# Kernel optimization log

Measured on AMD Instinct MI355X. Metric: run time of the kernel, lower is better.

Reference implementation:

```python
import jax, jax.numpy as jnp
import numpy as np

N, E, F, K = 20000, 320000, 256, 3


def setup_inputs() -> dict:
    key = jax.random.key(0)
    ks = jax.random.split(key, 10)
    x = jax.random.normal(ks[0], (N, F), jnp.float32)
    edge_index = jax.random.randint(ks[1], (2, E), 0, N)
    edge_weight = jax.random.uniform(ks[2], (E,), jnp.float32)
    h = jax.random.normal(ks[3], (N, F), jnp.float32)
    c = jax.random.normal(ks[4], (N, F), jnp.float32)
    s = 1.0 / np.sqrt(F)
    W = jax.random.normal(ks[5], (4, F, F), jnp.float32) * s        # x->gate (i,f,c,o)
    theta = jax.random.normal(ks[6], (4, K, F, F), jnp.float32) * s  # Cheb weights per gate
    b_conv = jnp.zeros((4, F), jnp.float32)                          # ChebConv biases
    b = jnp.zeros((4, F), jnp.float32)                               # gate biases
    w_c = jax.random.normal(ks[7], (3, F), jnp.float32) * s          # peephole (i,f,o)
    W_cls = jax.random.normal(ks[8], (F, 1), jnp.float32) * s
    b_cls = jnp.zeros((1,), jnp.float32)
    return dict(x=x, edge_index=edge_index, edge_weight=edge_weight, h=h, c=c,
                W=W, theta=theta, b_conv=b_conv, b=b, w_c=w_c, W_cls=W_cls, b_cls=b_cls)


def _cheb(h, src, dst, wnorm, theta_g, b_g):
    # ChebConv with sym normalization, lambda_max=2: L_hat = -D^{-1/2} A D^{-1/2}
    n = h.shape[0]

    def prop(v):  # (L_hat v)[dst] = sum_e wnorm[e] * v[src[e]]
        return jax.ops.segment_sum(wnorm[:, None] * v[src], dst, num_segments=n)

    Tx0 = h
    out = Tx0 @ theta_g[0]
    Tx1 = prop(h)
    out = out + Tx1 @ theta_g[1]
    for k in range(2, theta_g.shape[0]):
        Tx2 = 2.0 * prop(Tx1) - Tx0
        out = out + Tx2 @ theta_g[k]
        Tx0, Tx1 = Tx1, Tx2
    return out + b_g


def _gclstm(x, src, dst, wnorm, h, c, W, theta, b_conv, b, w_c):
    conv = lambda g: _cheb(h, src, dst, wnorm, theta[g], b_conv[g])
    i = jax.nn.sigmoid(x @ W[0] + conv(0) + w_c[0] * c + b[0])
    f = jax.nn.sigmoid(x @ W[1] + conv(1) + w_c[1] * c + b[1])
    t = jnp.tanh(x @ W[2] + conv(2) + b[2])
    c_new = f * c + i * t
    o = jax.nn.sigmoid(x @ W[3] + conv(3) + w_c[2] * c_new + b[3])
    h_new = o * jnp.tanh(c_new)
    return h_new, c_new


def reference(x, edge_index, edge_weight, h, c, W, theta, b_conv, b, w_c, W_cls, b_cls):
    src, dst = edge_index[0], edge_index[1]
    deg = jax.ops.segment_sum(edge_weight, src, num_segments=x.shape[0])
    dis = jnp.where(deg > 0, jax.lax.rsqrt(jnp.maximum(deg, 1e-12)), 0.0)
    wnorm = -dis[src] * edge_weight * dis[dst]
    h0, c0 = _gclstm(x, src, dst, wnorm, h, c, W, theta, b_conv, b, w_c)
    out = jax.nn.relu(h0) @ W_cls + b_cls  # [N, 1]
    return out, h0, c0
```

## Files before the change

### kernel.cpp

```cpp
#include <hip/hip_runtime.h>
#include <stdint.h>

#define FDIM 256
#define KDIM 1024

typedef __attribute__((ext_vector_type(8))) short short8;
typedef __attribute__((ext_vector_type(4))) float floatx4;

#define GLOBAL_AS __attribute__((address_space(1)))
#define LDS_AS    __attribute__((address_space(3)))

static __device__ __forceinline__ unsigned short f2bf(float f) {
    unsigned int u = __float_as_uint(f);
    unsigned int r = (u + 0x7FFFu + ((u >> 16) & 1u)) >> 16;
    return (unsigned short)r;
}
static __device__ __forceinline__ float bf2f(unsigned short s) {
    return __uint_as_float(((unsigned int)s) << 16);
}
static __device__ __forceinline__ float sig(float x) {
    return 1.f / (1.f + __expf(-x));
}


__global__ void k_degcnt(const int* __restrict__ src, const int* __restrict__ dst,
                         const float* __restrict__ ew, float* deg, int* cnt, int e) {
    int i = blockIdx.x * blockDim.x + threadIdx.x;
    if (i < e) {
        atomicAdd(&deg[src[i]], ew[i]);
        atomicAdd(&cnt[dst[i]], 1);
    }
}

__global__ void k_dis(const float* __restrict__ deg, float* __restrict__ dis, int n) {
    int i = blockIdx.x * blockDim.x + threadIdx.x;
    if (i < n) {
        float d = deg[i];
        dis[i] = d > 0.f ? rsqrtf(fmaxf(d, 1e-12f)) : 0.f;
    }
}

__launch_bounds__(1024)
__global__ void k_scan1(const int* __restrict__ cnt, int* __restrict__ offs,
                        int* __restrict__ part, int n) {
    __shared__ int wsum[16];
    int b = blockIdx.x;
    int i = b * 1024 + (int)threadIdx.x;
    int lane = threadIdx.x & 63;
    int wid = threadIdx.x >> 6;
    int x = (i < n) ? cnt[i] : 0;
#pragma unroll
    for (int s = 1; s < 64; s <<= 1) {
        int t = __shfl_up(x, s);
        if (lane >= s) x += t;
    }
    if (lane == 63) wsum[wid] = x;
    __syncthreads();
    if (wid == 0) {
        int y = (lane < 16) ? wsum[lane] : 0;
#pragma unroll
        for (int s = 1; s < 16; s <<= 1) {
            int t = __shfl_up(y, s);
            if (lane >= s) y += t;
        }
        if (lane < 16) wsum[lane] = y;
    }
    __syncthreads();
    int wbase = (wid > 0) ? wsum[wid - 1] : 0;
    if (i < n) offs[i + 1] = wbase + x;
    if (threadIdx.x == 1023) part[b] = wsum[15];
}

__launch_bounds__(1024)
__global__ void k_scan2(int* __restrict__ offs, const int* __restrict__ part, int n) {
    __shared__ int sprefix;
    int b = blockIdx.x;
    if (threadIdx.x < 64) {
        int p = ((int)threadIdx.x < b) ? part[threadIdx.x] : 0;
#pragma unroll
        for (int s = 32; s; s >>= 1) p += __shfl_down(p, s);
        if (threadIdx.x == 0) sprefix = p;
    }
    __syncthreads();
    int i = b * 1024 + (int)threadIdx.x;
    if (i < n) offs[i + 1] += sprefix;
    if (b == 0 && threadIdx.x == 0) offs[0] = 0;
}

__global__ void k_scatter(const int* __restrict__ src, const int* __restrict__ dst,
                          const float* __restrict__ ew, const float* __restrict__ dis,
                          const int* __restrict__ offs, int* cur,
                          int* __restrict__ csr_src, float* __restrict__ csr_w, int e) {
    int i = blockIdx.x * blockDim.x + threadIdx.x;
    if (i < e) {
        int s = src[i], d = dst[i];
        float wn = -dis[s] * ew[i] * dis[d];
        int pos = offs[d] + atomicAdd(&cur[d], 1);
        csr_src[pos] = s;
        csr_w[pos] = wn;
    }
}


__global__ void k_packA(const float* __restrict__ x, const float* __restrict__ h,
                        unsigned short* __restrict__ A, int n) {
    int t = blockIdx.x * blockDim.x + threadIdx.x;
    int node = t >> 6, q = t & 63;
    if (node >= n) return;
    floatx4 xv = *(const floatx4*)(x + (size_t)node * FDIM + q * 4);
    floatx4 hv = *(const floatx4*)(h + (size_t)node * FDIM + q * 4);
    ushort4 ox, oh;
    ox.x = f2bf(xv[0]); ox.y = f2bf(xv[1]); ox.z = f2bf(xv[2]); ox.w = f2bf(xv[3]);
    oh.x = f2bf(hv[0]); oh.y = f2bf(hv[1]); oh.z = f2bf(hv[2]); oh.w = f2bf(hv[3]);
    *(ushort4*)(A + (size_t)node * KDIM + q * 4) = ox;
    *(ushort4*)(A + (size_t)node * KDIM + FDIM + q * 4) = oh;
}

__global__ void k_packBt(const float* __restrict__ W, const float* __restrict__ theta,
                         unsigned short* __restrict__ Bt) {
    int t = blockIdx.x * blockDim.x + threadIdx.x;
    int p = t >> 10, r = t & 1023;
    int group = p >> 6, gate = (p >> 4) & 3;
    int feat = (group << 4) | (p & 15);
    int kb = r >> 8, rr = r & 255;
    float v;
    if (kb == 0) v = W[((size_t)(gate * FDIM + rr)) * FDIM + feat];
    else         v = theta[((size_t)((gate * 3 + (kb - 1)) * FDIM + rr)) * FDIM + feat];
    Bt[t] = f2bf(v);
}


__launch_bounds__(256)
__global__ void k_prop1(unsigned short* __restrict__ A, const int* __restrict__ offs,
                        const int* __restrict__ csr_src, const float* __restrict__ csr_w, int n) {
    int wid = (blockIdx.x * blockDim.x + threadIdx.x) >> 6;
    int lane = threadIdx.x & 63;
    if (wid >= n) return;
    int half = lane >> 5, l = lane & 31;
    int beg = offs[wid], end = offs[wid + 1];
    float a[8] = {0.f, 0.f, 0.f, 0.f, 0.f, 0.f, 0.f, 0.f};
    int j = beg + half;
    for (; j + 2 < end; j += 4) {
        int s0 = csr_src[j], s1 = csr_src[j + 2];
        float w0 = csr_w[j], w1 = csr_w[j + 2];
        short8 v0 = *(const short8*)(A + (size_t)s0 * KDIM + FDIM + l * 8);
        short8 v1 = *(const short8*)(A + (size_t)s1 * KDIM + FDIM + l * 8);
#pragma unroll
        for (int k = 0; k < 8; ++k)
            a[k] += w0 * bf2f((unsigned short)v0[k]) + w1 * bf2f((unsigned short)v1[k]);
    }
    if (j < end) {
        int s0 = csr_src[j];
        float w0 = csr_w[j];
        short8 v0 = *(const short8*)(A + (size_t)s0 * KDIM + FDIM + l * 8);
#pragma unroll
        for (int k = 0; k < 8; ++k) a[k] += w0 * bf2f((unsigned short)v0[k]);
    }
#pragma unroll
    for (int k = 0; k < 8; ++k) a[k] += __shfl_xor(a[k], 32);
    if (half == 0) {
        short8 o;
#pragma unroll
        for (int k = 0; k < 8; ++k) o[k] = (short)f2bf(a[k]);
        *(short8*)(A + (size_t)wid * KDIM + 2 * FDIM + l * 8) = o;
    }
}

__launch_bounds__(256)
__global__ void k_prop2(unsigned short* __restrict__ A, const float* __restrict__ h,
                        const int* __restrict__ offs,
                        const int* __restrict__ csr_src, const float* __restrict__ csr_w, int n) {
    int wid = (blockIdx.x * blockDim.x + threadIdx.x) >> 6;
    int lane = threadIdx.x & 63;
    if (wid >= n) return;
    int half = lane >> 5, l = lane & 31;
    int beg = offs[wid], end = offs[wid + 1];
    float a[8] = {0.f, 0.f, 0.f, 0.f, 0.f, 0.f, 0.f, 0.f};
    int j = beg + half;
    for (; j + 2 < end; j += 4) {
        int s0 = csr_src[j], s1 = csr_src[j + 2];
        float w0 = csr_w[j], w1 = csr_w[j + 2];
        short8 v0 = *(const short8*)(A + (size_t)s0 * KDIM + 2 * FDIM + l * 8);
        short8 v1 = *(const short8*)(A + (size_t)s1 * KDIM + 2 * FDIM + l * 8);
#pragma unroll
        for (int k = 0; k < 8; ++k)
            a[k] += w0 * bf2f((unsigned short)v0[k]) + w1 * bf2f((unsigned short)v1[k]);
    }
    if (j < end) {
        int s0 = csr_src[j];
        float w0 = csr_w[j];
        short8 v0 = *(const short8*)(A + (size_t)s0 * KDIM + 2 * FDIM + l * 8);
#pragma unroll
        for (int k = 0; k < 8; ++k) a[k] += w0 * bf2f((unsigned short)v0[k]);
    }
#pragma unroll
    for (int k = 0; k < 8; ++k) a[k] += __shfl_xor(a[k], 32);
    if (half == 0) {
        floatx4 hv0 = *(const floatx4*)(h + (size_t)wid * FDIM + l * 8);
        floatx4 hv1 = *(const floatx4*)(h + (size_t)wid * FDIM + l * 8 + 4);
        short8 o;
#pragma unroll
        for (int k = 0; k < 4; ++k) o[k] = (short)f2bf(2.f * a[k] - hv0[k]);
#pragma unroll
        for (int k = 0; k < 4; ++k) o[4 + k] = (short)f2bf(2.f * a[4 + k] - hv1[k]);
        *(short8*)(A + (size_t)wid * KDIM + 3 * FDIM + l * 8) = o;
    }
}


__launch_bounds__(256, 3)
__global__ void k_gemm(const unsigned short* __restrict__ A, const unsigned short* __restrict__ Bt,
                       const float* __restrict__ c, const float* __restrict__ b_conv,
                       const float* __restrict__ b, const float* __restrict__ w_c,
                       const float* __restrict__ Wcls,
                       float* __restrict__ out_h, float* __restrict__ out_c,
                       float* __restrict__ cls_part, int M, int mtiles) {
    __shared__ unsigned short sA[128 * 64];
    __shared__ unsigned short sB[128 * 64];
    int tid = threadIdx.x;
    int lane = tid & 63;
    int w = tid >> 6;
    int nb = mtiles * 8;
    int bid = blockIdx.x;
    int wg = (bid & 7) * (nb >> 3) + (bid >> 3);
    int mt = wg >> 3;
    int nt = wg & 7;
    int brow = mt * 128, bcol = nt * 128;
    int wr = (w >> 1) * 64, wc = (w & 1) * 64;
    int l15 = lane & 15, l4 = lane >> 4;

    floatx4 acc[4][4];
#pragma unroll
    for (int m = 0; m < 4; ++m)
#pragma unroll
        for (int g = 0; g < 4; ++g)
            acc[m][g] = (floatx4){0.f, 0.f, 0.f, 0.f};

    for (int kt = 0; kt < 16; ++kt) {
        int k0 = kt * 64;
#pragma unroll
        for (int p = 0; p < 4; ++p) {
            int cch = tid + p * 256;
            int row = cch >> 3, cslot = cch & 7;
            int csrc = cslot ^ (row & 7);
            int grow = brow + row; if (grow >= M) grow = M - 1;
            const unsigned short* g = A + (size_t)grow * KDIM + k0 + csrc * 8;
            __builtin_amdgcn_global_load_lds((const GLOBAL_AS void*)g,
                                             (LDS_AS void*)(sA + cch * 8), 16, 0, 0);
        }
#pragma unroll
        for (int p = 0; p < 4; ++p) {
            int cch = tid + p * 256;
            int row = cch >> 3, cslot = cch & 7;
            int csrc = cslot ^ (row & 7);
            const unsigned short* g = Bt + (size_t)(bcol + row) * KDIM + k0 + csrc * 8;
            __builtin_amdgcn_global_load_lds((const GLOBAL_AS void*)g,
                                             (LDS_AS void*)(sB + cch * 8), 16, 0, 0);
        }
        __syncthreads();

#pragma unroll
        for (int ks = 0; ks < 2; ++ks) {
            short8 af[4], bfr[4];
#pragma unroll
            for (int m = 0; m < 4; ++m) {
                int ra = wr + m * 16 + l15;
                af[m] = *(const short8*)(sA + ra * 64 + ((ks * 4 + l4) ^ (ra & 7)) * 8);
            }
#pragma unroll
            for (int g = 0; g < 4; ++g) {
                int rb = wc + g * 16 + l15;
                bfr[g] = *(const short8*)(sB + rb * 64 + ((ks * 4 + l4) ^ (rb & 7)) * 8);
            }
#pragma unroll
            for (int m = 0; m < 4; ++m)
#pragma unroll
                for (int g = 0; g < 4; ++g)
                    acc[m][g] = __builtin_amdgcn_mfma_f32_16x16x32_bf16(af[m], bfr[g], acc[m][g], 0, 0, 0);
        }
        __syncthreads();
    }

    int group = (bcol + wc) >> 6;
    int feat = (group << 4) | l15;
    float bc0 = b_conv[feat], bc1 = b_conv[FDIM + feat];
    float bc2 = b_conv[2 * FDIM + feat], bc3 = b_conv[3 * FDIM + feat];
    float bb0 = b[feat], bb1 = b[FDIM + feat];
    float bb2 = b[2 * FDIM + feat], bb3 = b[3 * FDIM + feat];
    float wci = w_c[feat], wcf = w_c[FDIM + feat], wco = w_c[2 * FDIM + feat];
    float wcl = Wcls[feat];

#pragma unroll
    for (int m = 0; m < 4; ++m) {
#pragma unroll
        for (int j = 0; j < 4; ++j) {
            int node = brow + wr + m * 16 + l4 * 4 + j;
            bool ok = node < M;
            int nidx = ok ? node : (M - 1);
            float cv = c[(size_t)nidx * FDIM + feat];
            float iv = sig(acc[m][0][j] + bc0 + wci * cv + bb0);
            float fv = sig(acc[m][1][j] + bc1 + wcf * cv + bb1);
            float tv = tanhf(acc[m][2][j] + bc2 + bb2);
            float cn = fv * cv + iv * tv;
            float ov = sig(acc[m][3][j] + bc3 + wco * cn + bb3);
            float hn = ov * tanhf(cn);
            if (ok) {
                out_h[(size_t)node * FDIM + feat] = hn;
                out_c[(size_t)node * FDIM + feat] = cn;
            }
            float pcls = fmaxf(hn, 0.f) * wcl;
#pragma unroll
            for (int s = 1; s < 16; s <<= 1) pcls += __shfl_xor(pcls, s);
            if (ok && l15 == 0) cls_part[(size_t)node * 16 + group] = pcls;
        }
    }
}

__global__ void k_cls(const float* __restrict__ cls_part, const float* __restrict__ bcls,
                      float* __restrict__ out_cls, int n) {
    int i = blockIdx.x * blockDim.x + threadIdx.x;
    if (i >= n) return;
    const floatx4* p = (const floatx4*)(cls_part + (size_t)i * 16);
    floatx4 v0 = p[0], v1 = p[1], v2 = p[2], v3 = p[3];
    float s = v0[0] + v0[1] + v0[2] + v0[3] + v1[0] + v1[1] + v1[2] + v1[3]
            + v2[0] + v2[1] + v2[2] + v2[3] + v3[0] + v3[1] + v3[2] + v3[3];
    out_cls[i] = s + bcls[0];
}


extern "C" void kernel_launch(void* const* d_in, const int* in_sizes, int n_in,
                              void* d_out, int out_size, void* d_ws, size_t ws_size,
                              hipStream_t stream) {
    const float* x      = (const float*)d_in[0];
    const int*   eidx   = (const int*)d_in[1];
    const float* ew     = (const float*)d_in[2];
    const float* h      = (const float*)d_in[3];
    const float* c      = (const float*)d_in[4];
    const float* W      = (const float*)d_in[5];
    const float* theta  = (const float*)d_in[6];
    const float* b_conv = (const float*)d_in[7];
    const float* b      = (const float*)d_in[8];
    const float* w_c    = (const float*)d_in[9];
    const float* Wcls   = (const float*)d_in[10];
    const float* bcls   = (const float*)d_in[11];

    const int N = in_sizes[0] / FDIM;
    const int E = in_sizes[2];
    const int* src = eidx;
    const int* dst = eidx + E;

    char* ws = (char*)d_ws;
    size_t off = 0;
    auto alloc = [&](size_t bytes) -> void* {
        void* p = ws + off;
        off += (bytes + 255) & ~(size_t)255;
        return p;
    };
    unsigned short* A   = (unsigned short*)alloc((size_t)N * KDIM * 2);
    unsigned short* Bt  = (unsigned short*)alloc((size_t)KDIM * KDIM * 2);
    float* cls_part     = (float*)alloc((size_t)N * 16 * 4);
    float* deg          = (float*)alloc((size_t)N * 4);
    int*   cnt          = (int*)alloc((size_t)N * 4);
    int*   cur          = (int*)alloc((size_t)N * 4);
    float* dis          = (float*)alloc((size_t)N * 4);
    int*   offs         = (int*)alloc((size_t)(N + 1) * 4);
    int*   part         = (int*)alloc(64 * 4);
    int*   csr_src      = (int*)alloc((size_t)E * 4);
    float* csr_w        = (float*)alloc((size_t)E * 4);
    (void)ws_size; (void)n_in; (void)out_size;

    float* out_cls = (float*)d_out;
    float* out_h   = out_cls + N;
    float* out_c   = out_h + (size_t)N * FDIM;

    size_t zbytes = (size_t)((char*)(cur + N) - (char*)deg);
    hipMemsetAsync(deg, 0, zbytes, stream);

    int nsb = (N + 1023) / 1024;
    k_degcnt<<<(E + 255) / 256, 256, 0, stream>>>(src, dst, ew, deg, cnt, E);
    k_dis<<<(N + 255) / 256, 256, 0, stream>>>(deg, dis, N);
    k_scan1<<<nsb, 1024, 0, stream>>>(cnt, offs, part, N);
    k_scan2<<<nsb, 1024, 0, stream>>>(offs, part, N);
    k_scatter<<<(E + 255) / 256, 256, 0, stream>>>(src, dst, ew, dis, offs, cur, csr_src, csr_w, E);
    k_packA<<<(N * 64 + 255) / 256, 256, 0, stream>>>(x, h, A, N);
    k_packBt<<<(KDIM * KDIM + 255) / 256, 256, 0, stream>>>(W, theta, Bt);
    k_prop1<<<(N * 64 + 255) / 256, 256, 0, stream>>>(A, offs, csr_src, csr_w, N);
    k_prop2<<<(N * 64 + 255) / 256, 256, 0, stream>>>(A, h, offs, csr_src, csr_w, N);
    int mtiles = (N + 127) / 128;
    k_gemm<<<mtiles * 8, 256, 0, stream>>>(A, Bt, c, b_conv, b, w_c, Wcls,
                                           out_h, out_c, cls_part, N, mtiles);
    k_cls<<<(N + 255) / 256, 256, 0, stream>>>(cls_part, bcls, out_cls, N);
}
```

Before: 200.6 us.

## Double-buffer GEMM LDS tiles, pack CSR as int2, unroll gathers, fold rsqrt into scatter

The GEMM kernel now stages the next K tile into a second LDS buffer while computing on the current one, using explicit vmcnt waits and raw barriers, and drops its occupancy hint from 3 to 2 blocks. Source index and weight are packed into one int2 CSR array so each edge is a single load. The prop kernels are unrolled to four gathers per half-wave. The separate dis kernel is removed and the rsqrt is computed inside the scatter. Together these aim to hide global-to-LDS latency and cut launch and memory traffic, at the cost of twice the LDS per block and lower occupancy in the GEMM.

```diff
diff --git a/kernel.cpp b/kernel.cpp
--- a/kernel.cpp
+++ b/kernel.cpp
@@ -29,14 +29,6 @@
     if (i < e) {
         atomicAdd(&deg[src[i]], ew[i]);
         atomicAdd(&cnt[dst[i]], 1);
-    }
-}
-
-__global__ void k_dis(const float* __restrict__ deg, float* __restrict__ dis, int n) {
-    int i = blockIdx.x * blockDim.x + threadIdx.x;
-    if (i < n) {
-        float d = deg[i];
-        dis[i] = d > 0.f ? rsqrtf(fmaxf(d, 1e-12f)) : 0.f;
     }
 }
 
@@ -88,16 +80,18 @@
 }
 
 __global__ void k_scatter(const int* __restrict__ src, const int* __restrict__ dst,
-                          const float* __restrict__ ew, const float* __restrict__ dis,
+                          const float* __restrict__ ew, const float* __restrict__ deg,
                           const int* __restrict__ offs, int* cur,
-                          int* __restrict__ csr_src, float* __restrict__ csr_w, int e) {
+                          int2* __restrict__ csr, int e) {
     int i = blockIdx.x * blockDim.x + threadIdx.x;
     if (i < e) {
         int s = src[i], d = dst[i];
-        float wn = -dis[s] * ew[i] * dis[d];
+        float ds_ = deg[s], dd = deg[d];
+        float rs = ds_ > 0.f ? rsqrtf(fmaxf(ds_, 1e-12f)) : 0.f;
+        float rd = dd > 0.f ? rsqrtf(fmaxf(dd, 1e-12f)) : 0.f;
+        float wn = -rs * ew[i] * rd;
         int pos = offs[d] + atomicAdd(&cur[d], 1);
-        csr_src[pos] = s;
-        csr_w[pos] = wn;
+        csr[pos] = make_int2(s, __float_as_int(wn));
     }
 }
 
@@ -132,7 +126,7 @@
 
 __launch_bounds__(256)
 __global__ void k_prop1(unsigned short* __restrict__ A, const int* __restrict__ offs,
-                        const int* __restrict__ csr_src, const float* __restrict__ csr_w, int n) {
+                        const int2* __restrict__ csr, int n) {
     int wid = (blockIdx.x * blockDim.x + threadIdx.x) >> 6;
     int lane = threadIdx.x & 63;
     if (wid >= n) return;
@@ -140,19 +134,23 @@
     int beg = offs[wid], end = offs[wid + 1];
     float a[8] = {0.f, 0.f, 0.f, 0.f, 0.f, 0.f, 0.f, 0.f};
     int j = beg + half;
-    for (; j + 2 < end; j += 4) {
-        int s0 = csr_src[j], s1 = csr_src[j + 2];
-        float w0 = csr_w[j], w1 = csr_w[j + 2];
-        short8 v0 = *(const short8*)(A + (size_t)s0 * KDIM + FDIM + l * 8);
-        short8 v1 = *(const short8*)(A + (size_t)s1 * KDIM + FDIM + l * 8);
+    for (; j + 6 < end; j += 8) {
+        int2 e0 = csr[j], e1 = csr[j + 2], e2 = csr[j + 4], e3 = csr[j + 6];
+        short8 v0 = *(const short8*)(A + (size_t)e0.x * KDIM + FDIM + l * 8);
+        short8 v1 = *(const short8*)(A + (size_t)e1.x * KDIM + FDIM + l * 8);
+        short8 v2 = *(const short8*)(A + (size_t)e2.x * KDIM + FDIM + l * 8);
+        short8 v3 = *(const short8*)(A + (size_t)e3.x * KDIM + FDIM + l * 8);
+        float w0 = __int_as_float(e0.y), w1 = __int_as_float(e1.y);
+        float w2 = __int_as_float(e2.y), w3 = __int_as_float(e3.y);
 #pragma unroll
         for (int k = 0; k < 8; ++k)
-            a[k] += w0 * bf2f((unsigned short)v0[k]) + w1 * bf2f((unsigned short)v1[k]);
-    }
-    if (j < end) {
-        int s0 = csr_src[j];
-        float w0 = csr_w[j];
-        short8 v0 = *(const short8*)(A + (size_t)s0 * KDIM + FDIM + l * 8);
+            a[k] += w0 * bf2f((unsigned short)v0[k]) + w1 * bf2f((unsigned short)v1[k])
+                  + w2 * bf2f((unsigned short)v2[k]) + w3 * bf2f((unsigned short)v3[k]);
+    }
+    for (; j < end; j += 2) {
+        int2 e0 = csr[j];
+        float w0 = __int_as_float(e0.y);
+        short8 v0 = *(const short8*)(A + (size_t)e0.x * KDIM + FDIM + l * 8);
 #pragma unroll
         for (int k = 0; k < 8; ++k) a[k] += w0 * bf2f((unsigned short)v0[k]);
     }
@@ -168,8 +166,7 @@
 
 __launch_bounds__(256)
 __global__ void k_prop2(unsigned short* __restrict__ A, const float* __restrict__ h,
-                        const int* __restrict__ offs,
-                        const int* __restrict__ csr_src, const float* __restrict__ csr_w, int n) {
+                        const int* __restrict__ offs, const int2* __restrict__ csr, int n) {
     int wid = (blockIdx.x * blockDim.x + threadIdx.x) >> 6;
     int lane = threadIdx.x & 63;
     if (wid >= n) return;
@@ -177,19 +174,23 @@
     int beg = offs[wid], end = offs[wid + 1];
     float a[8] = {0.f, 0.f, 0.f, 0.f, 0.f, 0.f, 0.f, 0.f};
     int j = beg + half;
-    for (; j + 2 < end; j += 4) {
-        int s0 = csr_src[j], s1 = csr_src[j + 2];
-        float w0 = csr_w[j], w1 = csr_w[j + 2];
-        short8 v0 = *(const short8*)(A + (size_t)s0 * KDIM + 2 * FDIM + l * 8);
-        short8 v1 = *(const short8*)(A + (size_t)s1 * KDIM + 2 * FDIM + l * 8);
+    for (; j + 6 < end; j += 8) {
+        int2 e0 = csr[j], e1 = csr[j + 2], e2 = csr[j + 4], e3 = csr[j + 6];
+        short8 v0 = *(const short8*)(A + (size_t)e0.x * KDIM + 2 * FDIM + l * 8);
+        short8 v1 = *(const short8*)(A + (size_t)e1.x * KDIM + 2 * FDIM + l * 8);
+        short8 v2 = *(const short8*)(A + (size_t)e2.x * KDIM + 2 * FDIM + l * 8);
+        short8 v3 = *(const short8*)(A + (size_t)e3.x * KDIM + 2 * FDIM + l * 8);
+        float w0 = __int_as_float(e0.y), w1 = __int_as_float(e1.y);
+        float w2 = __int_as_float(e2.y), w3 = __int_as_float(e3.y);
 #pragma unroll
         for (int k = 0; k < 8; ++k)
-            a[k] += w0 * bf2f((unsigned short)v0[k]) + w1 * bf2f((unsigned short)v1[k]);
-    }
-    if (j < end) {
-        int s0 = csr_src[j];
-        float w0 = csr_w[j];
-        short8 v0 = *(const short8*)(A + (size_t)s0 * KDIM + 2 * FDIM + l * 8);
+            a[k] += w0 * bf2f((unsigned short)v0[k]) + w1 * bf2f((unsigned short)v1[k])
+                  + w2 * bf2f((unsigned short)v2[k]) + w3 * bf2f((unsigned short)v3[k]);
+    }
+    for (; j < end; j += 2) {
+        int2 e0 = csr[j];
+        float w0 = __int_as_float(e0.y);
+        short8 v0 = *(const short8*)(A + (size_t)e0.x * KDIM + 2 * FDIM + l * 8);
 #pragma unroll
         for (int k = 0; k < 8; ++k) a[k] += w0 * bf2f((unsigned short)v0[k]);
     }
@@ -208,15 +209,15 @@
 }
 
 
-__launch_bounds__(256, 3)
+__launch_bounds__(256, 2)
 __global__ void k_gemm(const unsigned short* __restrict__ A, const unsigned short* __restrict__ Bt,
                        const float* __restrict__ c, const float* __restrict__ b_conv,
                        const float* __restrict__ b, const float* __restrict__ w_c,
                        const float* __restrict__ Wcls,
                        float* __restrict__ out_h, float* __restrict__ out_c,
                        float* __restrict__ cls_part, int M, int mtiles) {
-    __shared__ unsigned short sA[128 * 64];
-    __shared__ unsigned short sB[128 * 64];
+    __shared__ unsigned short sA[2][128 * 64];
+    __shared__ unsigned short sB[2][128 * 64];
     int tid = threadIdx.x;
     int lane = tid & 63;
     int w = tid >> 6;
@@ -229,14 +230,7 @@
     int wr = (w >> 1) * 64, wc = (w & 1) * 64;
     int l15 = lane & 15, l4 = lane >> 4;
 
-    floatx4 acc[4][4];
-#pragma unroll
-    for (int m = 0; m < 4; ++m)
-#pragma unroll
-        for (int g = 0; g < 4; ++g)
-            acc[m][g] = (floatx4){0.f, 0.f, 0.f, 0.f};
-
-    for (int kt = 0; kt < 16; ++kt) {
+    auto STAGE = [&](int kt, int bufi) {
         int k0 = kt * 64;
 #pragma unroll
         for (int p = 0; p < 4; ++p) {
@@ -246,7 +240,7 @@
             int grow = brow + row; if (grow >= M) grow = M - 1;
             const unsigned short* g = A + (size_t)grow * KDIM + k0 + csrc * 8;
             __builtin_amdgcn_global_load_lds((const GLOBAL_AS void*)g,
-                                             (LDS_AS void*)(sA + cch * 8), 16, 0, 0);
+                                             (LDS_AS void*)(sA[bufi] + cch * 8), 16, 0, 0);
         }
 #pragma unroll
         for (int p = 0; p < 4; ++p) {
@@ -255,9 +249,29 @@
             int csrc = cslot ^ (row & 7);
             const unsigned short* g = Bt + (size_t)(bcol + row) * KDIM + k0 + csrc * 8;
             __builtin_amdgcn_global_load_lds((const GLOBAL_AS void*)g,
-                                             (LDS_AS void*)(sB + cch * 8), 16, 0, 0);
-        }
-        __syncthreads();
+                                             (LDS_AS void*)(sB[bufi] + cch * 8), 16, 0, 0);
+        }
+    };
+
+    floatx4 acc[4][4];
+#pragma unroll
+    for (int m = 0; m < 4; ++m)
+#pragma unroll
+        for (int g = 0; g < 4; ++g)
+            acc[m][g] = (floatx4){0.f, 0.f, 0.f, 0.f};
+
+    STAGE(0, 0);
+
+    for (int kt = 0; kt < 16; ++kt) {
+        int cur = kt & 1;
+        if (kt < 15) {
+            STAGE(kt + 1, cur ^ 1);
+            asm volatile("s_waitcnt vmcnt(8)" ::: "memory");
+        } else {
+            asm volatile("s_waitcnt vmcnt(0)" ::: "memory");
+        }
+        __builtin_amdgcn_s_barrier();
+        __builtin_amdgcn_sched_barrier(0);
 
 #pragma unroll
         for (int ks = 0; ks < 2; ++ks) {
@@ -265,12 +279,12 @@
 #pragma unroll
             for (int m = 0; m < 4; ++m) {
                 int ra = wr + m * 16 + l15;
-                af[m] = *(const short8*)(sA + ra * 64 + ((ks * 4 + l4) ^ (ra & 7)) * 8);
+                af[m] = *(const short8*)(sA[cur] + ra * 64 + ((ks * 4 + l4) ^ (ra & 7)) * 8);
             }
 #pragma unroll
             for (int g = 0; g < 4; ++g) {
                 int rb = wc + g * 16 + l15;
-                bfr[g] = *(const short8*)(sB + rb * 64 + ((ks * 4 + l4) ^ (rb & 7)) * 8);
+                bfr[g] = *(const short8*)(sB[cur] + rb * 64 + ((ks * 4 + l4) ^ (rb & 7)) * 8);
             }
 #pragma unroll
             for (int m = 0; m < 4; ++m)
@@ -278,7 +292,9 @@
                 for (int g = 0; g < 4; ++g)
                     acc[m][g] = __builtin_amdgcn_mfma_f32_16x16x32_bf16(af[m], bfr[g], acc[m][g], 0, 0, 0);
         }
-        __syncthreads();
+        asm volatile("s_waitcnt lgkmcnt(0)" ::: "memory");
+        __builtin_amdgcn_sched_barrier(0);
+        __builtin_amdgcn_s_barrier();
     }
 
     int group = (bcol + wc) >> 6;
@@ -362,11 +378,9 @@
     float* deg          = (float*)alloc((size_t)N * 4);
     int*   cnt          = (int*)alloc((size_t)N * 4);
     int*   cur          = (int*)alloc((size_t)N * 4);
-    float* dis          = (float*)alloc((size_t)N * 4);
     int*   offs         = (int*)alloc((size_t)(N + 1) * 4);
     int*   part         = (int*)alloc(64 * 4);
-    int*   csr_src      = (int*)alloc((size_t)E * 4);
-    float* csr_w        = (float*)alloc((size_t)E * 4);
+    int2*  csr          = (int2*)alloc((size_t)E * 8);
     (void)ws_size; (void)n_in; (void)out_size;
 
     float* out_cls = (float*)d_out;
@@ -378,14 +392,13 @@
 
     int nsb = (N + 1023) / 1024;
     k_degcnt<<<(E + 255) / 256, 256, 0, stream>>>(src, dst, ew, deg, cnt, E);
-    k_dis<<<(N + 255) / 256, 256, 0, stream>>>(deg, dis, N);
     k_scan1<<<nsb, 1024, 0, stream>>>(cnt, offs, part, N);
     k_scan2<<<nsb, 1024, 0, stream>>>(offs, part, N);
-    k_scatter<<<(E + 255) / 256, 256, 0, stream>>>(src, dst, ew, dis, offs, cur, csr_src, csr_w, E);
+    k_scatter<<<(E + 255) / 256, 256, 0, stream>>>(src, dst, ew, deg, offs, cur, csr, E);
     k_packA<<<(N * 64 + 255) / 256, 256, 0, stream>>>(x, h, A, N);
     k_packBt<<<(KDIM * KDIM + 255) / 256, 256, 0, stream>>>(W, theta, Bt);
-    k_prop1<<<(N * 64 + 255) / 256, 256, 0, stream>>>(A, offs, csr_src, csr_w, N);
-    k_prop2<<<(N * 64 + 255) / 256, 256, 0, stream>>>(A, h, offs, csr_src, csr_w, N);
+    k_prop1<<<(N * 64 + 255) / 256, 256, 0, stream>>>(A, offs, csr, N);
+    k_prop2<<<(N * 64 + 255) / 256, 256, 0, stream>>>(A, h, offs, csr, N);
     int mtiles = (N + 127) / 128;
     k_gemm<<<mtiles * 8, 256, 0, stream>>>(A, Bt, c, b_conv, b, w_c, Wcls,
                                            out_h, out_c, cls_part, N, mtiles);
```

Result: slower. 211.7 us (+5.6%).
